# Optimization experiments

Measured on AMD Instinct MI355X. Metric: run time of the kernel, lower is better.

The kernel has to match this reference:

```python
import jax, jax.numpy as jnp
import numpy as np

QMAX = 127.0
QMIN = -128.0
THRESHOLD = 5e-07

def setup_inputs() -> dict:
    key = jax.random.key(0)
    k1, k2, k3 = jax.random.split(key, 3)
    B, S, Din, Dout = 4, 2048, 4096, 4096
    x = jax.random.normal(k1, (B, S, Din), dtype=jnp.float32)
    # Emulate QuantizedLinear.__init__: per-output-channel symmetric int8 weight quant
    w_fp = jax.random.normal(k2, (Dout, Din), dtype=jnp.float32) * 0.02
    w_scale = jnp.clip(jnp.max(jnp.abs(w_fp), axis=1, keepdims=True), THRESHOLD, None) / QMAX  # [Dout,1]
    weight = jnp.round(w_fp / w_scale)  # int8-valued, stored float32, [Dout, Din]
    weight_scale = w_scale.reshape(1, 1, Dout)  # [1,1,Dout]
    bias = jax.random.normal(k3, (Dout,), dtype=jnp.float32) * 0.01
    return {"x": x, "weight": weight, "weight_scale": weight_scale, "bias": bias}

def reference(x, weight, weight_scale, bias):
    # Dynamic per-tensor activation quantization (act_quant=True, no fixed range)
    fp_min = jnp.min(x)
    fp_max = jnp.max(x)
    scale = (fp_max - fp_min) / (QMAX - QMIN)
    zero_point = jnp.clip(jnp.round(QMIN - fp_min / scale), QMIN, QMAX)
    q_input = jnp.round(x / scale + zero_point)  # int8-valued float
    # F.linear(q_input - zp, weight): [B,S,Din] x [Dout,Din]^T -> [B,S,Dout]
    y = jnp.einsum('bsd,od->bso', q_input - zero_point, weight)
    y = y * scale * weight_scale  # dequant epilogue (weight_scale broadcasts [1,1,Dout])
    return y + bias
```

## Files before the change

### kernel.cpp

```cpp
#include <hip/hip_runtime.h>
#include <hip/hip_bf16.h>
#include <stdint.h>

typedef __attribute__((ext_vector_type(4))) int i32x4;

#define K_DIM 4096
#define M_DIM 8192
#define N_DIM 4096

#define BM 256
#define BN 256
#define BKB 128
#define K_TILES (K_DIM / BKB)
#define GITERS (K_TILES / 2)

__device__ __forceinline__ void gload_lds16(const void* g, void* l) {
    __builtin_amdgcn_global_load_lds(
        (__attribute__((address_space(1))) void*)(void*)g,
        (__attribute__((address_space(3))) void*)(void*)l,
        16, 0, 0);
}

__global__ void mmcw_kernel(const float* __restrict__ x, long n4,
                            float* __restrict__ partials,
                            const float* __restrict__ w,
                            signed char* __restrict__ Wq,
                            int* __restrict__ rowsum) {
    if (blockIdx.x < 1024) {
        const float4* x4 = (const float4*)x;
        float mn = 1e30f, mx = -1e30f;
        long stride = (long)1024 * blockDim.x;
        for (long i = (long)blockIdx.x * blockDim.x + threadIdx.x; i < n4; i += stride) {
            float4 v = x4[i];
            mn = fminf(mn, fminf(fminf(v.x, v.y), fminf(v.z, v.w)));
            mx = fmaxf(mx, fmaxf(fmaxf(v.x, v.y), fmaxf(v.z, v.w)));
        }
        #pragma unroll
        for (int off = 32; off; off >>= 1) {
            mn = fminf(mn, __shfl_down(mn, off));
            mx = fmaxf(mx, __shfl_down(mx, off));
        }
        __shared__ float smn[4], smx[4];
        int wid = threadIdx.x >> 6, lane = threadIdx.x & 63;
        if (lane == 0) { smn[wid] = mn; smx[wid] = mx; }
        __syncthreads();
        if (threadIdx.x == 0) {
            mn = fminf(fminf(smn[0], smn[1]), fminf(smn[2], smn[3]));
            mx = fmaxf(fmaxf(smx[0], smx[1]), fmaxf(smx[2], smx[3]));
            partials[blockIdx.x] = mn;
            partials[1024 + blockIdx.x] = mx;
        }
    } else {
        int row = (blockIdx.x - 1024) * 4 + (threadIdx.x >> 6);
        int lane = threadIdx.x & 63;
        const float4* src = (const float4*)(w + (long)row * K_DIM);
        uint4* dst = (uint4*)(Wq + (long)row * K_DIM);
        float s = 0.f;
        #pragma unroll
        for (int k = 0; k < 4; k++) {
            int u = k * 64 + lane;
            unsigned wrd[4];
            #pragma unroll
            for (int j = 0; j < 4; j++) {
                float4 v = src[u * 4 + j];
                float e[4] = {v.x, v.y, v.z, v.w};
                unsigned word = 0;
                #pragma unroll
                for (int b = 0; b < 4; b++) {
                    int iv = (int)e[b];
                    s += e[b];
                    word |= ((unsigned)iv & 0xffu) << (8 * b);
                }
                wrd[j] = word;
            }
            uint4 o; o.x = wrd[0]; o.y = wrd[1]; o.z = wrd[2]; o.w = wrd[3];
            dst[u] = o;
        }
        #pragma unroll
        for (int off = 32; off; off >>= 1) s += __shfl_down(s, off);
        if (lane == 0) rowsum[row] = (int)s;
    }
}

__global__ void finalize_fold_kernel(const float* __restrict__ partials,
                                     const int* __restrict__ rowsum,
                                     const float* __restrict__ wscale,
                                     const float* __restrict__ bias,
                                     float* __restrict__ scal,
                                     float* __restrict__ outscale,
                                     float* __restrict__ bias2) {
    float mn = 1e30f, mx = -1e30f;
    for (int i = threadIdx.x; i < 1024; i += 256) {
        mn = fminf(mn, partials[i]);
        mx = fmaxf(mx, partials[1024 + i]);
    }
    #pragma unroll
    for (int off = 32; off; off >>= 1) {
        mn = fminf(mn, __shfl_down(mn, off));
        mx = fmaxf(mx, __shfl_down(mx, off));
    }
    __shared__ float smn[4], smx[4];
    __shared__ float s_scale, s_zp;
    int wid = threadIdx.x >> 6, lane = threadIdx.x & 63;
    if (lane == 0) { smn[wid] = mn; smx[wid] = mx; }
    __syncthreads();
    if (threadIdx.x == 0) {
        mn = fminf(fminf(smn[0], smn[1]), fminf(smn[2], smn[3]));
        mx = fmaxf(fmaxf(smx[0], smx[1]), fmaxf(smx[2], smx[3]));
        float scale = (mx - mn) / 255.0f;
        float zp = rintf(-128.0f - mn / scale);
        zp = fminf(fmaxf(zp, -128.0f), 127.0f);
        scal[0] = scale;
        scal[1] = zp;
        s_scale = scale; s_zp = zp;
    }
    __syncthreads();
    float scale = s_scale, zp = s_zp;
    for (int i = threadIdx.x; i < 4096; i += 256) {
        float os = scale * wscale[i];
        outscale[i] = os;
        bias2[i] = bias[i] - zp * (float)rowsum[i] * os;
    }
}

__global__ void quantize_kernel(const float* __restrict__ x,
                                const float* __restrict__ scal,
                                uint4* __restrict__ q, long n16) {
    float scale = scal[0];
    float zp = scal[1];
    long stride = (long)gridDim.x * blockDim.x;
    for (long i = (long)blockIdx.x * blockDim.x + threadIdx.x; i < n16; i += stride) {
        const float4* xp = (const float4*)x + i * 4;
        unsigned wrd[4];
        #pragma unroll
        for (int w = 0; w < 4; w++) {
            float4 v = xp[w];
            float e[4] = {v.x, v.y, v.z, v.w};
            unsigned word = 0;
            #pragma unroll
            for (int j = 0; j < 4; j++) {
                float qf = rintf(e[j] / scale + zp);
                qf = fminf(fmaxf(qf, -128.0f), 127.0f);
                int iq = (int)qf;
                word |= ((unsigned)iq & 0xffu) << (8 * j);
            }
            wrd[w] = word;
        }
        uint4 o; o.x = wrd[0]; o.y = wrd[1]; o.z = wrd[2]; o.w = wrd[3];
        q[i] = o;
    }
}

__global__ __launch_bounds__(512, 2) void gemm_kernel(
    const signed char* __restrict__ A,
    const signed char* __restrict__ W,
    const float* __restrict__ outscale,
    const float* __restrict__ bias2,
    float* __restrict__ C) {
    extern __shared__ char lds[];
    char* As = lds;
    char* Bs = lds + 65536;

    int nwg = gridDim.x;
    int cpx = nwg >> 3;
    int bid = blockIdx.x;
    int wg = (bid & 7) * cpx + (bid >> 3);
    int tm = wg >> 4;
    int tn = wg & 15;
    int m0 = tm * BM, n0 = tn * BN;

    int t = threadIdx.x;
    int wid = t >> 6, lane = t & 63;
    int wr = wid >> 2, wc = wid & 3;
    int lr = lane & 15, lk = lane >> 4;
    int ksw0 = (lk ^ (lr & 7)) * 16;
    int ksw1 = ((4 + lk) ^ (lr & 7)) * 16;

    int R0 = t >> 3;
    int csw = ((t & 7) ^ ((t >> 3) & 7)) * 16;
    const signed char* aSrc = A + (long)(m0 + R0) * K_DIM + csw;
    const signed char* bSrc = W + (long)(n0 + ((R0 >> 5) << 6) + (R0 & 31)) * K_DIM + csw;
    int ldd = t * 16;

#define STAGE_A(BUF, UN, KT) do { \
    const signed char* _s = aSrc + (long)(UN) * 64 * K_DIM + (long)(KT) * BKB; \
    char* _d = As + (BUF) * 32768 + (UN) * 16384 + ldd; \
    gload_lds16(_s, _d); \
    gload_lds16(_s + (long)128 * K_DIM, _d + 8192); } while (0)

#define STAGE_B(BUF, UN, KT) do { \
    const signed char* _s = bSrc + (long)(UN) * 32 * K_DIM + (long)(KT) * BKB; \
    char* _d = Bs + (BUF) * 32768 + (UN) * 16384 + ldd; \
    gload_lds16(_s, _d); \
    gload_lds16(_s + (long)128 * K_DIM, _d + 8192); } while (0)

#define READ_A(BUF, MH) do { \
    const char* _p = As + (BUF) * 32768 + (MH) * 16384 + (wr * 64 + lr) * 128; \
    _Pragma("unroll") \
    for (int _mm = 0; _mm < 4; ++_mm) { \
        a[_mm * 2]     = *(const i32x4*)(_p + _mm * 2048 + ksw0); \
        a[_mm * 2 + 1] = *(const i32x4*)(_p + _mm * 2048 + ksw1); } } while (0)

#define READ_B(BUF, NH, BR) do { \
    const char* _p = Bs + (BUF) * 32768 + (NH) * 16384 + (wc * 32 + lr) * 128; \
    _Pragma("unroll") \
    for (int _nn = 0; _nn < 2; ++_nn) { \
        BR[_nn * 2]     = *(const i32x4*)(_p + _nn * 2048 + ksw0); \
        BR[_nn * 2 + 1] = *(const i32x4*)(_p + _nn * 2048 + ksw1); } } while (0)

#define MFMA_QUAD(MH, NH, BR) do { \
    _Pragma("unroll") \
    for (int _mm = 0; _mm < 4; ++_mm) \
    _Pragma("unroll") \
    for (int _nn = 0; _nn < 2; ++_nn) { \
        acc[(MH) * 4 + _mm][(NH) * 2 + _nn] = __builtin_amdgcn_mfma_i32_16x16x64_i8( \
            a[_mm * 2], BR[_nn * 2], acc[(MH) * 4 + _mm][(NH) * 2 + _nn], 0, 0, 0); \
        acc[(MH) * 4 + _mm][(NH) * 2 + _nn] = __builtin_amdgcn_mfma_i32_16x16x64_i8( \
            a[_mm * 2 + 1], BR[_nn * 2 + 1], acc[(MH) * 4 + _mm][(NH) * 2 + _nn], 0, 0, 0); } } while (0)

#define BAR()   asm volatile("s_barrier" ::: "memory")
#define LGKM0() asm volatile("s_waitcnt lgkmcnt(0)" ::: "memory")
#define LGKM8() asm volatile("s_waitcnt lgkmcnt(8)" ::: "memory")
#define VM6()   asm volatile("s_waitcnt vmcnt(6)" ::: "memory")
#define VM0()   asm volatile("s_waitcnt vmcnt(0)" ::: "memory")
#define PRIO1() __builtin_amdgcn_s_setprio(1)
#define PRIO0() __builtin_amdgcn_s_setprio(0)

    i32x4 acc[8][4];
    #pragma unroll
    for (int i = 0; i < 8; i++)
        #pragma unroll
        for (int j = 0; j < 4; j++)
            acc[i][j] = (i32x4){0, 0, 0, 0};

    i32x4 a[8], b0[4], b1[4];

    STAGE_A(0, 0, 0); STAGE_B(0, 0, 0); STAGE_B(0, 1, 0); STAGE_A(0, 1, 0);
    STAGE_A(1, 0, 1); STAGE_B(1, 0, 1); STAGE_B(1, 1, 1);
    VM6();
    BAR();

    for (int it = 0; it < GITERS; ++it) {
        int t1 = 2 * it + 1;
        int tn0 = 2 * it + 2, tn1 = 2 * it + 3;
        bool st = (it < GITERS - 1);

        READ_A(0, 0);
        READ_B(0, 0, b0);
        STAGE_A(1, 1, t1);
        LGKM8();
        BAR(); LGKM0();
        PRIO1(); MFMA_QUAD(0, 0, b0); PRIO0();
        BAR();

        READ_B(0, 1, b1);
        if (st) STAGE_A(0, 0, tn0);
        BAR(); LGKM0();
        PRIO1(); MFMA_QUAD(0, 1, b1); PRIO0();
        BAR();

        READ_A(0, 1);
        if (st) STAGE_B(0, 0, tn0);
        BAR(); LGKM0();
        PRIO1(); MFMA_QUAD(1, 1, b1); PRIO0();
        BAR();

        if (st) { STAGE_B(0, 1, tn0); VM6(); } else { VM0(); }
        BAR();
        PRIO1(); MFMA_QUAD(1, 0, b0); PRIO0();
        BAR();

        READ_A(1, 0);
        READ_B(1, 0, b0);
        if (st) STAGE_A(0, 1, tn0);
        LGKM8();
        BAR(); LGKM0();
        PRIO1(); MFMA_QUAD(0, 0, b0); PRIO0();
        BAR();

        READ_B(1, 1, b1);
        if (st) STAGE_A(1, 0, tn1);
        BAR(); LGKM0();
        PRIO1(); MFMA_QUAD(0, 1, b1); PRIO0();
        BAR();

        READ_A(1, 1);
        if (st) STAGE_B(1, 0, tn1);
        BAR(); LGKM0();
        PRIO1(); MFMA_QUAD(1, 1, b1); PRIO0();
        BAR();

        if (st) { STAGE_B(1, 1, tn1); VM6(); }
        BAR();
        PRIO1(); MFMA_QUAD(1, 0, b0); PRIO0();
        BAR();
    }

    #pragma unroll
    for (int j = 0; j < 4; j++) {
        int col = n0 + wc * 64 + j * 16 + lr;
        float os = outscale[col];
        float bs = bias2[col];
        #pragma unroll
        for (int i = 0; i < 8; i++) {
            int rbase = m0 + wr * 128 + i * 16 + lk * 4;
            #pragma unroll
            for (int r = 0; r < 4; r++) {
                C[(long)(rbase + r) * N_DIM + col] = (float)acc[i][j][r] * os + bs;
            }
        }
    }
#undef STAGE_A
#undef STAGE_B
#undef READ_A
#undef READ_B
#undef MFMA_QUAD
}

extern "C" void kernel_launch(void* const* d_in, const int* in_sizes, int n_in,
                              void* d_out, int out_size, void* d_ws, size_t ws_size,
                              hipStream_t stream) {
    const float* x      = (const float*)d_in[0];
    const float* weight = (const float*)d_in[1];
    const float* wscale = (const float*)d_in[2];
    const float* bias   = (const float*)d_in[3];
    float* out = (float*)d_out;

    char* ws = (char*)d_ws;
    signed char* Aq = (signed char*)ws;
    signed char* Wq = (signed char*)(ws + (size_t)32 * 1024 * 1024);
    float* partials = (float*)(ws + (size_t)48 * 1024 * 1024);
    float* scal     = partials + 2048;
    int*   rowsum   = (int*)(scal + 16);
    float* outsc    = (float*)(rowsum + 4096);
    float* bias2    = outsc + 4096;

    long n_x = (long)M_DIM * K_DIM;

    mmcw_kernel<<<2048, 256, 0, stream>>>(x, n_x / 4, partials, weight, Wq, rowsum);
    finalize_fold_kernel<<<1, 256, 0, stream>>>(partials, rowsum, wscale, bias,
                                                scal, outsc, bias2);
    quantize_kernel<<<2048, 256, 0, stream>>>(x, scal, (uint4*)Aq, n_x / 16);

    int lds_bytes = 131072;
    (void)hipFuncSetAttribute((const void*)gemm_kernel,
                              hipFuncAttributeMaxDynamicSharedMemorySize,
                              lds_bytes);
    dim3 grid((M_DIM / BM) * (N_DIM / BN));
    gemm_kernel<<<grid, 512, lds_bytes, stream>>>(Aq, Wq, outsc, bias2, out);
}
```

Measured before the change: 200.1 us.

## Double-buffer LDS register fragments to overlap ds_reads with MFMA phases

Adds a second A-fragment register set and rotates the B-fragment buffers so that each LDS read for the next MFMA quad is issued one phase ahead and overlaps the current quad's MFMAs. The explicit lgkmcnt waits are removed, leaving the compiler to insert dependency waits. The prologue now waits for all global loads and preloads the first fragments. This raises register pressure, and the correctness of the rotated buffer usage and barrier placement becomes more delicate.

```diff
diff --git a/kernel.cpp b/kernel.cpp
--- a/kernel.cpp
+++ b/kernel.cpp
@@ -194,12 +194,12 @@
     gload_lds16(_s, _d); \
     gload_lds16(_s + (long)128 * K_DIM, _d + 8192); } while (0)
 
-#define READ_A(BUF, MH) do { \
+#define READ_A(BUF, MH, AR) do { \
     const char* _p = As + (BUF) * 32768 + (MH) * 16384 + (wr * 64 + lr) * 128; \
     _Pragma("unroll") \
     for (int _mm = 0; _mm < 4; ++_mm) { \
-        a[_mm * 2]     = *(const i32x4*)(_p + _mm * 2048 + ksw0); \
-        a[_mm * 2 + 1] = *(const i32x4*)(_p + _mm * 2048 + ksw1); } } while (0)
+        AR[_mm * 2]     = *(const i32x4*)(_p + _mm * 2048 + ksw0); \
+        AR[_mm * 2 + 1] = *(const i32x4*)(_p + _mm * 2048 + ksw1); } } while (0)
 
 #define READ_B(BUF, NH, BR) do { \
     const char* _p = Bs + (BUF) * 32768 + (NH) * 16384 + (wc * 32 + lr) * 128; \
@@ -208,19 +208,17 @@
         BR[_nn * 2]     = *(const i32x4*)(_p + _nn * 2048 + ksw0); \
         BR[_nn * 2 + 1] = *(const i32x4*)(_p + _nn * 2048 + ksw1); } } while (0)
 
-#define MFMA_QUAD(MH, NH, BR) do { \
+#define MFMA_QUAD(MH, NH, AR, BR) do { \
     _Pragma("unroll") \
     for (int _mm = 0; _mm < 4; ++_mm) \
     _Pragma("unroll") \
     for (int _nn = 0; _nn < 2; ++_nn) { \
         acc[(MH) * 4 + _mm][(NH) * 2 + _nn] = __builtin_amdgcn_mfma_i32_16x16x64_i8( \
-            a[_mm * 2], BR[_nn * 2], acc[(MH) * 4 + _mm][(NH) * 2 + _nn], 0, 0, 0); \
+            AR[_mm * 2], BR[_nn * 2], acc[(MH) * 4 + _mm][(NH) * 2 + _nn], 0, 0, 0); \
         acc[(MH) * 4 + _mm][(NH) * 2 + _nn] = __builtin_amdgcn_mfma_i32_16x16x64_i8( \
-            a[_mm * 2 + 1], BR[_nn * 2 + 1], acc[(MH) * 4 + _mm][(NH) * 2 + _nn], 0, 0, 0); } } while (0)
+            AR[_mm * 2 + 1], BR[_nn * 2 + 1], acc[(MH) * 4 + _mm][(NH) * 2 + _nn], 0, 0, 0); } } while (0)
 
 #define BAR()   asm volatile("s_barrier" ::: "memory")
-#define LGKM0() asm volatile("s_waitcnt lgkmcnt(0)" ::: "memory")
-#define LGKM8() asm volatile("s_waitcnt lgkmcnt(8)" ::: "memory")
 #define VM6()   asm volatile("s_waitcnt vmcnt(6)" ::: "memory")
 #define VM0()   asm volatile("s_waitcnt vmcnt(0)" ::: "memory")
 #define PRIO1() __builtin_amdgcn_s_setprio(1)
@@ -233,66 +231,68 @@
         for (int j = 0; j < 4; j++)
             acc[i][j] = (i32x4){0, 0, 0, 0};
 
-    i32x4 a[8], b0[4], b1[4];
+    i32x4 aA[8], aB[8], b0[4], b1[4];
 
     STAGE_A(0, 0, 0); STAGE_B(0, 0, 0); STAGE_B(0, 1, 0); STAGE_A(0, 1, 0);
     STAGE_A(1, 0, 1); STAGE_B(1, 0, 1); STAGE_B(1, 1, 1);
-    VM6();
+    VM0();
     BAR();
+    READ_A(0, 0, aA);
+    READ_B(0, 0, b1);
 
     for (int it = 0; it < GITERS; ++it) {
         int t1 = 2 * it + 1;
         int tn0 = 2 * it + 2, tn1 = 2 * it + 3;
         bool st = (it < GITERS - 1);
 
-        READ_A(0, 0);
-        READ_B(0, 0, b0);
+        READ_B(0, 1, b0);
         STAGE_A(1, 1, t1);
-        LGKM8();
-        BAR(); LGKM0();
-        PRIO1(); MFMA_QUAD(0, 0, b0); PRIO0();
-        BAR();
-
-        READ_B(0, 1, b1);
+        BAR();
+        PRIO1(); MFMA_QUAD(0, 0, aA, b1); PRIO0();
+        BAR();
+
+        READ_A(0, 1, aB);
         if (st) STAGE_A(0, 0, tn0);
-        BAR(); LGKM0();
-        PRIO1(); MFMA_QUAD(0, 1, b1); PRIO0();
-        BAR();
-
-        READ_A(0, 1);
+        BAR();
+        PRIO1(); MFMA_QUAD(0, 1, aA, b0); PRIO0();
+        BAR();
+
         if (st) STAGE_B(0, 0, tn0);
-        BAR(); LGKM0();
-        PRIO1(); MFMA_QUAD(1, 1, b1); PRIO0();
+        BAR();
+        PRIO1(); MFMA_QUAD(1, 1, aB, b0); PRIO0();
         BAR();
 
         if (st) { STAGE_B(0, 1, tn0); VM6(); } else { VM0(); }
         BAR();
-        PRIO1(); MFMA_QUAD(1, 0, b0); PRIO0();
-        BAR();
-
-        READ_A(1, 0);
+        READ_A(1, 0, aA);
         READ_B(1, 0, b0);
+        PRIO1(); MFMA_QUAD(1, 0, aB, b1); PRIO0();
+        BAR();
+
+        READ_B(1, 1, b1);
         if (st) STAGE_A(0, 1, tn0);
-        LGKM8();
-        BAR(); LGKM0();
-        PRIO1(); MFMA_QUAD(0, 0, b0); PRIO0();
-        BAR();
-
-        READ_B(1, 1, b1);
+        BAR();
+        PRIO1(); MFMA_QUAD(0, 0, aA, b0); PRIO0();
+        BAR();
+
+        READ_A(1, 1, aB);
         if (st) STAGE_A(1, 0, tn1);
-        BAR(); LGKM0();
-        PRIO1(); MFMA_QUAD(0, 1, b1); PRIO0();
-        BAR();
-
-        READ_A(1, 1);
+        BAR();
+        PRIO1(); MFMA_QUAD(0, 1, aA, b1); PRIO0();
+        BAR();
+
         if (st) STAGE_B(1, 0, tn1);
-        BAR(); LGKM0();
-        PRIO1(); MFMA_QUAD(1, 1, b1); PRIO0();
+        BAR();
+        PRIO1(); MFMA_QUAD(1, 1, aB, b1); PRIO0();
         BAR();
 
         if (st) { STAGE_B(1, 1, tn1); VM6(); }
         BAR();
-        PRIO1(); MFMA_QUAD(1, 0, b0); PRIO0();
+        if (st) {
+            READ_A(0, 0, aA);
+            READ_B(0, 0, b1);
+        }
+        PRIO1(); MFMA_QUAD(1, 0, aB, b0); PRIO0();
         BAR();
     }
 
```

Measured after the change: 210.3 us. 5.1% more time.
